# Optimization experiments

Hardware: AMD Instinct MI355X
Metric: run time of the kernel (lower is better)

Reference implementation:

```python
import jax, jax.numpy as jnp
import numpy as np

NODE_TYPES = ('user', 'vn', 'tag', 'staff', 'producer', 'character', 'trait')
N = {'user': 100000, 'vn': 40000, 'tag': 3000, 'staff': 20000, 'producer': 8000, 'character': 60000, 'trait': 3000}
# (src_type, dst_type) per edge type, in HGATConfig.edge_types order
EDGE_TYPES = (('user','vn'), ('vn','user'), ('vn','tag'), ('tag','vn'), ('vn','staff'), ('staff','vn'),
              ('vn','staff'), ('staff','vn'), ('vn','producer'), ('producer','vn'), ('vn','character'),
              ('character','vn'), ('character','trait'), ('trait','character'))
E_COUNTS = (1000000, 1000000, 500000, 500000, 200000, 200000, 200000, 200000, 100000, 100000, 300000, 300000, 400000, 400000)
HID = 128
LAYERS = 3
# number of edge types targeting each node type (HeteroConv aggr='mean' divisor)
NUM_DST = {'user': 1, 'vn': 6, 'tag': 1, 'staff': 2, 'producer': 1, 'character': 2, 'trait': 1}


def _l2norm(x):
    n = jnp.linalg.norm(x, axis=-1, keepdims=True)
    return x / jnp.maximum(n, 1e-12)


def _layernorm(x, g, b):
    m = jnp.mean(x, axis=-1, keepdims=True)
    v = jnp.mean((x - m) ** 2, axis=-1, keepdims=True)
    return (x - m) * jax.lax.rsqrt(v + 1e-5) * g + b


def _forward(xs, Wp, bp, Wl, bl, Wr, ln_g, ln_b, Wu, bu, Wv, bv, eis):
    # input projection per node type
    h = {t: xs[t] @ Wp[i].T + bp[i] for i, t in enumerate(NODE_TYPES)}
    # inverse in-degree per edge type (constant across layers)
    inv_deg = []
    for e, (st, dt) in enumerate(EDGE_TYPES):
        dst = eis[e][1]
        deg = jax.ops.segment_sum(jnp.ones(dst.shape[0], jnp.float32), dst, num_segments=N[dt])
        inv_deg.append(1.0 / jnp.maximum(deg, 1.0))
    for l in range(LAYERS):
        acc = {t: jnp.zeros((N[t], HID), h[t].dtype) for t in NODE_TYPES}
        for e, (st, dt) in enumerate(EDGE_TYPES):
            src, dst = eis[e][0], eis[e][1]
            # SAGEConv: mean-aggregate neighbor feats, then lin_l(agg) + lin_r(root), L2-normalize
            agg = jax.ops.segment_sum(h[st][src], dst, num_segments=N[dt]) * inv_deg[e][:, None]
            out = agg @ Wl[l, e].T + bl[l, e] + h[dt] @ Wr[l, e].T
            acc[dt] = acc[dt] + _l2norm(out)
        new_h = {}
        for i, t in enumerate(NODE_TYPES):
            x = acc[t] / NUM_DST[t] + h[t]  # HeteroConv mean over edge types + residual
            new_h[t] = jax.nn.relu(_layernorm(x, ln_g[l, i], ln_b[l, i]))  # dropout = identity (eval)
        h = new_h
    user_emb = _l2norm(h['user'] @ Wu.T + bu)
    vn_emb = _l2norm(h['vn'] @ Wv.T + bv)
    return user_emb, vn_emb


def setup_inputs() -> dict:
    key = jax.random.key(0)
    ks = iter(jax.random.split(key, 80))
    inp = {}
    for t in NODE_TYPES:
        inp['x_' + t] = jax.random.normal(next(ks), (N[t], HID), jnp.float32)
    for e, (st, dt) in enumerate(EDGE_TYPES):
        src = jax.random.randint(next(ks), (E_COUNTS[e],), 0, N[st], jnp.int32)
        dst = jax.random.randint(next(ks), (E_COUNTS[e],), 0, N[dt], jnp.int32)
        inp['ei_%d' % e] = jnp.stack([src, dst])
    s = 1.0 / np.sqrt(HID)
    inp['Wp'] = jax.random.normal(next(ks), (7, HID, HID), jnp.float32) * s
    inp['bp'] = jnp.zeros((7, HID), jnp.float32)
    inp['Wl'] = jax.random.normal(next(ks), (LAYERS, 14, HID, HID), jnp.float32) * s
    inp['bl'] = jnp.zeros((LAYERS, 14, HID), jnp.float32)
    inp['Wr'] = jax.random.normal(next(ks), (LAYERS, 14, HID, HID), jnp.float32) * s
    inp['ln_g'] = jnp.ones((LAYERS, 7, HID), jnp.float32)
    inp['ln_b'] = jnp.zeros((LAYERS, 7, HID), jnp.float32)
    inp['Wu'] = jax.random.normal(next(ks), (HID, HID), jnp.float32) * s
    inp['bu'] = jnp.zeros((HID,), jnp.float32)
    inp['Wv'] = jax.random.normal(next(ks), (HID, HID), jnp.float32) * s
    inp['bv'] = jnp.zeros((HID,), jnp.float32)
    return inp


def reference(x_user, x_vn, x_tag, x_staff, x_producer, x_character, x_trait,
              ei_0, ei_1, ei_2, ei_3, ei_4, ei_5, ei_6, ei_7, ei_8, ei_9, ei_10, ei_11, ei_12, ei_13,
              Wp, bp, Wl, bl, Wr, ln_g, ln_b, Wu, bu, Wv, bv):
    xs = {'user': x_user, 'vn': x_vn, 'tag': x_tag, 'staff': x_staff,
          'producer': x_producer, 'character': x_character, 'trait': x_trait}
    eis = [ei_0, ei_1, ei_2, ei_3, ei_4, ei_5, ei_6, ei_7, ei_8, ei_9, ei_10, ei_11, ei_12, ei_13]
    return _forward(xs, Wp, bp, Wl, bl, Wr, ln_g, ln_b, Wu, bu, Wv, bv, eis)
```

## Files before the change

### kernel.cpp

```cpp
#include <hip/hip_runtime.h>
#include <math.h>

#define TOTE 5400000
#define TOTN 234000
#define TOTC 514000
#define HID  128

#define NBUK 499
#define NBLK 1024


typedef __attribute__((ext_vector_type(8))) short short8;
typedef __attribute__((ext_vector_type(8))) __bf16 bf16x8;
typedef __attribute__((ext_vector_type(4))) float floatx4;
typedef __attribute__((ext_vector_type(2))) float float2v;

__constant__ int c_EPRE[15]   = {0,1000000,2000000,2500000,3000000,3200000,3400000,3600000,3800000,3900000,4000000,4300000,4600000,5000000,5400000};
__constant__ int c_ECNT[14]   = {1000000,1000000,500000,500000,200000,200000,200000,200000,100000,100000,300000,300000,400000,400000};
__constant__ int c_CNTOFF[14] = {0,40000,140000,143000,183000,203000,243000,263000,303000,311000,351000,411000,451000,454000};
__constant__ int c_CNTN[14]   = {40000,100000,3000,40000,20000,40000,20000,40000,8000,40000,60000,40000,3000,60000};
__constant__ int c_SRCOFF[14] = {0,100000,100000,140000,100000,143000,100000,143000,100000,163000,100000,171000,171000,231000};
__constant__ int c_NODEPRE[8] = {0,100000,140000,143000,163000,171000,231000,234000};
__constant__ int c_BSH[14]   = {9,10,6,10,10,11,10,11,10,11,11,11,6,11};
__constant__ int c_BBASE[15] = {0,79,177,224,264,284,304,324,344,352,372,402,422,469,499};

static __device__ __forceinline__ unsigned short f2bf(float f) {
    unsigned u = __float_as_uint(f);
    u = u + 0x7FFFu + ((u >> 16) & 1u);
    return (unsigned short)(u >> 16);
}
static __device__ __forceinline__ float bf2f(unsigned short s) {
    return __uint_as_float(((unsigned)s) << 16);
}

struct EdgeArgs { const int* ei[14]; };


__global__ __launch_bounds__(256) void hist_k(EdgeArgs a, int* __restrict__ blkHist) {
    __shared__ int h[NBUK];
    int t = threadIdx.x;
    for (int i = t; i < NBUK; i += 256) h[i] = 0;
    __syncthreads();
    const int per = (TOTE + NBLK - 1) / NBLK;
    int s = blockIdx.x * per;
    int eEnd = min(s + per, TOTE);
    for (int g = s + t; g < eEnd; g += 256) {
        int e = 0;
        while (g >= c_EPRE[e + 1]) e++;
        int k = g - c_EPRE[e];
        int dst = a.ei[e][c_ECNT[e] + k];
        atomicAdd(&h[c_BBASE[e] + (dst >> c_BSH[e])], 1);
    }
    __syncthreads();
    for (int i = t; i < NBUK; i += 256) blkHist[(size_t)i * NBLK + blockIdx.x] = h[i];
}

__global__ __launch_bounds__(256) void scan_blk_k(int* __restrict__ blkHist, int* __restrict__ bktCnt) {
    int b = blockIdx.x;
    int* p = blkHist + (size_t)b * NBLK;
    int t = threadIdx.x;
    int4 v = *(int4*)&p[t * 4];
    int s = v.x + v.y + v.z + v.w;
    int lane = t & 63, w = t >> 6;
    __shared__ int wt[4];
    int incl = s;
    #pragma unroll
    for (int d = 1; d < 64; d <<= 1) { int o = __shfl_up(incl, d); if (lane >= d) incl += o; }
    if (lane == 63) wt[w] = incl;
    __syncthreads();
    int wb = 0;
    for (int i = 0; i < w; i++) wb += wt[i];
    int excl = incl - s + wb;
    int4 o;
    o.x = excl; o.y = excl + v.x; o.z = excl + v.x + v.y; o.w = excl + v.x + v.y + v.z;
    *(int4*)&p[t * 4] = o;
    if (t == 255) bktCnt[b] = excl + s;
}

__global__ __launch_bounds__(512) void scans2_k(const int* __restrict__ bktCnt, int* __restrict__ bktEdgeBase) {
    int t = threadIdx.x;
    int v = (t < NBUK) ? bktCnt[t] : 0;
    int lane = t & 63, w = t >> 6;
    __shared__ int wt[8];
    int incl = v;
    #pragma unroll
    for (int d = 1; d < 64; d <<= 1) { int o = __shfl_up(incl, d); if (lane >= d) incl += o; }
    if (lane == 63) wt[w] = incl;
    __syncthreads();
    int wb = 0;
    for (int i = 0; i < w; i++) wb += wt[i];
    int excl = incl - v + wb;
    if (t < NBUK) bktEdgeBase[t] = excl;
    if (t == NBUK - 1) bktEdgeBase[NBUK] = excl + v;
}

__global__ __launch_bounds__(256) void scatter_k(EdgeArgs a, const int* __restrict__ blkHist,
        const int* __restrict__ bktEdgeBase, unsigned* __restrict__ pool) {
    __shared__ int cur[NBUK];
    int t = threadIdx.x;
    for (int i = t; i < NBUK; i += 256)
        cur[i] = bktEdgeBase[i] + blkHist[(size_t)i * NBLK + blockIdx.x];
    __syncthreads();
    const int per = (TOTE + NBLK - 1) / NBLK;
    int s = blockIdx.x * per;
    int eEnd = min(s + per, TOTE);
    for (int g = s + t; g < eEnd; g += 256) {
        int e = 0;
        while (g >= c_EPRE[e + 1]) e++;
        int k = g - c_EPRE[e];
        int src = a.ei[e][k];
        int dst = a.ei[e][c_ECNT[e] + k];
        int sh = c_BSH[e];
        unsigned rec = ((unsigned)(dst & ((1 << sh) - 1)) << 18) | (unsigned)(c_SRCOFF[e] + src);
        int p = atomicAdd(&cur[c_BBASE[e] + (dst >> sh)], 1);
        pool[p] = rec;
    }
}

__global__ __launch_bounds__(256) void csrfill_k(
        const unsigned* __restrict__ pool, const int* __restrict__ bktEdgeBase,
        int* __restrict__ cnt, int* __restrict__ cursor, float* __restrict__ invdeg,
        int* __restrict__ col) {
    __shared__ int hist[2048];
    __shared__ int cur[2048];
    __shared__ int wtot[4];
    __shared__ int wbase[4];
    int b = blockIdx.x;
    int t = threadIdx.x;
    int e = 0;
    while (b >= c_BBASE[e + 1]) e++;
    int lb = b - c_BBASE[e];
    int sh = c_BSH[e];
    int s0t = lb << sh;
    int span = min(1 << sh, c_CNTN[e] - s0t);
    int gs0 = c_CNTOFF[e] + s0t;
    int ebase = bktEdgeBase[b];
    int nrec = bktEdgeBase[b + 1] - ebase;

    for (int i = t; i < span; i += 256) hist[i] = 0;
    __syncthreads();
    for (int i = t; i < nrec; i += 256) atomicAdd(&hist[pool[ebase + i] >> 18], 1);
    __syncthreads();
    int base = t * 8, loc = 0, lv[8];
    #pragma unroll
    for (int i = 0; i < 8; i++) {
        int ii = base + i;
        int v = (ii < span) ? hist[ii] : 0;
        lv[i] = loc; loc += v;
    }
    int lane = t & 63, w = t >> 6;
    int incl = loc;
    #pragma unroll
    for (int d = 1; d < 64; d <<= 1) { int o = __shfl_up(incl, d); if (lane >= d) incl += o; }
    if (lane == 63) wtot[w] = incl;
    __syncthreads();
    if (t == 0) { int s2 = 0; for (int i = 0; i < 4; i++) { wbase[i] = s2; s2 += wtot[i]; } }
    __syncthreads();
    int texcl = incl - loc + wbase[w];
    #pragma unroll
    for (int i = 0; i < 8; i++) {
        int ii = base + i;
        if (ii < span) cur[ii] = texcl + lv[i];
    }
    __syncthreads();
    for (int i = t; i < span; i += 256) {
        int c = hist[i];
        cnt[gs0 + i] = c;
        cursor[gs0 + i] = ebase + cur[i] + c;
        invdeg[gs0 + i] = 1.0f / fmaxf((float)c, 1.0f);
    }
    __syncthreads();
    for (int i = t; i < nrec; i += 256) {
        unsigned rec = pool[ebase + i];
        int p = atomicAdd(&cur[rec >> 18], 1);
        col[ebase + p] = (int)(rec & 0x3FFFFu);
    }
}

struct XArgs { const float* x[7]; };
__global__ __launch_bounds__(256) void convx_k(XArgs a, unsigned short* __restrict__ hbf) {
    int i4 = blockIdx.x * 256 + threadIdx.x;
    if (i4 >= TOTN * 32) return;
    int idx = i4 * 4;
    int t = 0;
    while (idx >= c_NODEPRE[t + 1] * 128) t++;
    float4 v = *(const float4*)&a.x[t][idx - c_NODEPRE[t] * 128];
    uint2 p;
    p.x = (unsigned)f2bf(v.x) | ((unsigned)f2bf(v.y) << 16);
    p.y = (unsigned)f2bf(v.z) | ((unsigned)f2bf(v.w) << 16);
    *(uint2*)&hbf[idx] = p;
}

struct WArgs { const float* Wp; const float* Wl; const float* Wr; const float* Wu; const float* Wv; };
__global__ __launch_bounds__(256) void convw_k(WArgs a, unsigned short* __restrict__ wbf) {
    int i4 = blockIdx.x * 256 + threadIdx.x;
    if (i4 >= 93 * 4096) return;
    int idx = i4 * 4;
    int m = idx >> 14;
    int i = idx & 16383;
    const float* src;
    if (m < 7)       src = a.Wp + (size_t)m * 16384;
    else if (m < 49) src = a.Wl + (size_t)(m - 7) * 16384;
    else if (m < 91) src = a.Wr + (size_t)(m - 49) * 16384;
    else if (m == 91) src = a.Wu;
    else              src = a.Wv;
    float4 v = *(const float4*)&src[i];
    uint2 p;
    p.x = (unsigned)f2bf(v.x) | ((unsigned)f2bf(v.y) << 16);
    p.y = (unsigned)f2bf(v.z) | ((unsigned)f2bf(v.w) << 16);
    *(uint2*)&wbf[idx] = p;
}

#define ACC8v(u) do { \
    v01 += (float2v){__uint_as_float((u).x << 16), __uint_as_float((u).x & 0xFFFF0000u)}; \
    v23 += (float2v){__uint_as_float((u).y << 16), __uint_as_float((u).y & 0xFFFF0000u)}; \
    v45 += (float2v){__uint_as_float((u).z << 16), __uint_as_float((u).z & 0xFFFF0000u)}; \
    v67 += (float2v){__uint_as_float((u).w << 16), __uint_as_float((u).w & 0xFFFF0000u)}; } while (0)

__global__ __launch_bounds__(256) void agg_k(
        const int* __restrict__ cnt, const int* __restrict__ cursor,
        const float* __restrict__ inv_deg, const int* __restrict__ col,
        const unsigned short* __restrict__ hbf, unsigned short* __restrict__ slotb) {
    int row = blockIdx.x * 4 + (threadIdx.x >> 6);
    if (row >= TOTC) return;
    int lane = threadIdx.x & 63;
    int q = lane >> 4, li = lane & 15;
    int nn = cnt[row];
    int rs = cursor[row] - nn;
    const int* cp = col + rs;
    float2v v01 = {0.f, 0.f}, v23 = {0.f, 0.f}, v45 = {0.f, 0.f}, v67 = {0.f, 0.f};
    int j = 0;
    if (j + 8 <= nn) {
        int c0 = cp[q], c1 = cp[4 + q];
        for (; j + 8 <= nn; ) {
            int jn = j + 8;
            int n0 = 0, n1 = 0;
            if (jn + 8 <= nn) { n0 = cp[jn + q]; n1 = cp[jn + 4 + q]; }
            uint4 u0 = *(const uint4*)&hbf[(c0 << 7) + li * 8];
            uint4 u1 = *(const uint4*)&hbf[(c1 << 7) + li * 8];
            ACC8v(u0);
            ACC8v(u1);
            c0 = n0; c1 = n1; j = jn;
        }
    }
    for (; j < nn; j += 4) {
        if (j + q < nn) {
            int c = cp[j + q] << 7;
            uint4 u = *(const uint4*)&hbf[c + li * 8];
            ACC8v(u);
        }
    }
    float inv = inv_deg[row];
    float v[8] = {v01.x, v01.y, v23.x, v23.y, v45.x, v45.y, v67.x, v67.y};
    #pragma unroll
    for (int i = 0; i < 8; i++) {
        v[i] += __shfl_xor(v[i], 16);
        v[i] += __shfl_xor(v[i], 32);
        v[i] *= inv;
    }
    if (q == 0) {
        uint4 o;
        o.x = (unsigned)f2bf(v[0]) | ((unsigned)f2bf(v[1]) << 16);
        o.y = (unsigned)f2bf(v[2]) | ((unsigned)f2bf(v[3]) << 16);
        o.z = (unsigned)f2bf(v[4]) | ((unsigned)f2bf(v[5]) << 16);
        o.w = (unsigned)f2bf(v[6]) | ((unsigned)f2bf(v[7]) << 16);
        *(uint4*)&slotb[(size_t)row * HID + li * 8] = o;
    }
}

struct FusArgs {
    int blockPrefix[8];
    int ns[7];
    int a1off[7][6];
    const unsigned short* W1[7][6];
    const unsigned short* W2[7][6];
    const float* bias[7][6];
    int nodepre[7];
    int nrows[7];
    float invnd[7];
};

__global__ __launch_bounds__(256) void fusedln_k(FusArgs g,
        unsigned short* __restrict__ hbf, const unsigned short* __restrict__ slotb,
        const float* __restrict__ ln_g, const float* __restrict__ ln_b, int l) {
    __shared__ short As2[64 * 168];
    __shared__ short A1c[64 * 40];
    __shared__ short W1c[128 * 40];
    __shared__ short W2c[128 * 40];
    int b = blockIdx.x;
    int t = 0;
    while (b >= g.blockPrefix[t + 1]) t++;
    int nrows = g.nrows[t];
    int row0 = (b - g.blockPrefix[t]) * 64;
    int dst0 = g.nodepre[t] + row0;
    int tid = threadIdx.x;
    int w = tid >> 6, lane = tid & 63;
    int q = lane >> 4, m15 = lane & 15;

    {
        const uint4* h4 = (const uint4*)hbf;
        #pragma unroll
        for (int it = 0; it < 4; it++) {
            int c = tid + it * 256;
            int row = c >> 4, kc = c & 15;
            uint4 v = make_uint4(0u, 0u, 0u, 0u);
            if (row0 + row < nrows) v = h4[(size_t)(dst0 + row) * 16 + kc];
            *(uint4*)&As2[row * 168 + (kc >> 2) * 40 + (kc & 3) * 8] = v;
        }
    }

    floatx4 accsum[8];
    #pragma unroll
    for (int bb = 0; bb < 8; bb++) accsum[bb] = (floatx4){0.f, 0.f, 0.f, 0.f};

    int ns = g.ns[t];
    for (int ei = 0; ei < ns; ei++) {
        const uint4* A14 = (const uint4*)(slotb + (size_t)g.a1off[t][ei] * HID);
        const uint4* W14 = (const uint4*)g.W1[t][ei];
        const uint4* W24 = (const uint4*)g.W2[t][ei];
        floatx4 acc[8];
        #pragma unroll
        for (int bb = 0; bb < 8; bb++) acc[bb] = (floatx4){0.f, 0.f, 0.f, 0.f};
        for (int k0 = 0; k0 < 4; k0++) {
            __syncthreads();
            {
                int row = tid >> 2, kc = tid & 3;
                uint4 v = make_uint4(0u, 0u, 0u, 0u);
                if (row0 + row < nrows) v = A14[(size_t)(row0 + row) * 16 + k0 * 4 + kc];
                *(uint4*)&A1c[row * 40 + kc * 8] = v;
            }
            #pragma unroll
            for (int i = 0; i < 2; i++) {
                int idx = tid + i * 256;
                int c = idx >> 2, kc = idx & 3;
                *(uint4*)&W1c[c * 40 + kc * 8] = W14[(size_t)c * 16 + k0 * 4 + kc];
                *(uint4*)&W2c[c * 40 + kc * 8] = W24[(size_t)c * 16 + k0 * 4 + kc];
            }
            __syncthreads();
            bf16x8 a1 = __builtin_bit_cast(bf16x8, *(const short8*)&A1c[(w * 16 + m15) * 40 + q * 8]);
            bf16x8 a2 = __builtin_bit_cast(bf16x8, *(const short8*)&As2[(w * 16 + m15) * 168 + k0 * 40 + q * 8]);
            #pragma unroll
            for (int bb = 0; bb < 8; bb++) {
                bf16x8 w1 = __builtin_bit_cast(bf16x8, *(const short8*)&W1c[(bb * 16 + m15) * 40 + q * 8]);
                bf16x8 w2 = __builtin_bit_cast(bf16x8, *(const short8*)&W2c[(bb * 16 + m15) * 40 + q * 8]);
                acc[bb] = __builtin_amdgcn_mfma_f32_16x16x32_bf16(a1, w1, acc[bb], 0, 0, 0);
                acc[bb] = __builtin_amdgcn_mfma_f32_16x16x32_bf16(a2, w2, acc[bb], 0, 0, 0);
            }
        }
        const float* bias = g.bias[t][ei];
        #pragma unroll
        for (int bb = 0; bb < 8; bb++) {
            float bv = bias[bb * 16 + m15];
            #pragma unroll
            for (int reg = 0; reg < 4; reg++) acc[bb][reg] += bv;
        }
        #pragma unroll
        for (int reg = 0; reg < 4; reg++) {
            float ss = 0.f;
            #pragma unroll
            for (int bb = 0; bb < 8; bb++) ss += acc[bb][reg] * acc[bb][reg];
            ss += __shfl_xor(ss, 1);
            ss += __shfl_xor(ss, 2);
            ss += __shfl_xor(ss, 4);
            ss += __shfl_xor(ss, 8);
            float sc = 1.0f / fmaxf(sqrtf(ss), 1e-12f);
            #pragma unroll
            for (int bb = 0; bb < 8; bb++) accsum[bb][reg] += acc[bb][reg] * sc;
        }
    }

    float invnd = g.invnd[t];
    const float* gg = ln_g + ((size_t)l * 7 + t) * HID;
    const float* bbp = ln_b + ((size_t)l * 7 + t) * HID;
    float gv[8], bv2[8];
    #pragma unroll
    for (int bb = 0; bb < 8; bb++) {
        gv[bb]  = gg[bb * 16 + m15];
        bv2[bb] = bbp[bb * 16 + m15];
    }
    #pragma unroll
    for (int reg = 0; reg < 4; reg++) {
        int lrow = w * 16 + q * 4 + reg;
        float x[8];
        #pragma unroll
        for (int bb = 0; bb < 8; bb++) {
            float resid = bf2f((unsigned short)As2[lrow * 168 + (bb >> 1) * 40 + (bb & 1) * 16 + m15]);
            x[bb] = accsum[bb][reg] * invnd + resid;
        }
        float s = 0.f;
        #pragma unroll
        for (int bb = 0; bb < 8; bb++) s += x[bb];
        s += __shfl_xor(s, 1);
        s += __shfl_xor(s, 2);
        s += __shfl_xor(s, 4);
        s += __shfl_xor(s, 8);
        float mean = s * (1.0f / 128.0f);
        float vs = 0.f;
        #pragma unroll
        for (int bb = 0; bb < 8; bb++) { float d = x[bb] - mean; vs += d * d; }
        vs += __shfl_xor(vs, 1);
        vs += __shfl_xor(vs, 2);
        vs += __shfl_xor(vs, 4);
        vs += __shfl_xor(vs, 8);
        float rstd = rsqrtf(vs * (1.0f / 128.0f) + 1e-5f);
        if (row0 + lrow < nrows) {
            unsigned short* o = hbf + (size_t)(dst0 + lrow) * HID;
            #pragma unroll
            for (int bb = 0; bb < 8; bb++) {
                float y = (x[bb] - mean) * rstd * gv[bb] + bv2[bb];
                o[bb * 16 + m15] = f2bf(fmaxf(y, 0.f));
            }
        }
    }
}

struct GemmArgs {
    int blockPrefix[15];
    const unsigned short* A1[14];
    const unsigned short* W1[14];
    const float* bias[14]; void* out[14];
    int rows[14];
};

template<int MODE>
__global__ __launch_bounds__(256) void gemm_k(GemmArgs g) {
    __shared__ short As[64 * 40];
    __shared__ short Ws[128 * 40];
    int b = blockIdx.x;
    int s = 0;
    while (b >= g.blockPrefix[s + 1]) s++;
    int rows = g.rows[s];
    int row0 = (b - g.blockPrefix[s]) * 64;
    int t = threadIdx.x;
    int w = t >> 6, lane = t & 63;
    int q = lane >> 4, m15 = lane & 15;

    floatx4 acc[8];
    #pragma unroll
    for (int bb = 0; bb < 8; bb++) acc[bb] = (floatx4){0.f, 0.f, 0.f, 0.f};

    const uint4* A4 = (const uint4*)g.A1[s];
    const uint4* W4 = (const uint4*)g.W1[s];
    for (int k0 = 0; k0 < 128; k0 += 32) {
        __syncthreads();
        {
            int row = t >> 2, kc = t & 3;
            uint4 v = make_uint4(0u, 0u, 0u, 0u);
            if (row0 + row < rows) v = A4[(size_t)(row0 + row) * 16 + (k0 >> 3) + kc];
            *(uint4*)&As[row * 40 + kc * 8] = v;
        }
        #pragma unroll
        for (int i = 0; i < 2; i++) {
            int idx = t + i * 256;
            int c = idx >> 2, kc = idx & 3;
            uint4 v = W4[(size_t)c * 16 + (k0 >> 3) + kc];
            *(uint4*)&Ws[c * 40 + kc * 8] = v;
        }
        __syncthreads();
        bf16x8 af = __builtin_bit_cast(bf16x8, *(const short8*)&As[(w * 16 + m15) * 40 + q * 8]);
        #pragma unroll
        for (int bb = 0; bb < 8; bb++) {
            bf16x8 bf = __builtin_bit_cast(bf16x8, *(const short8*)&Ws[(bb * 16 + m15) * 40 + q * 8]);
            acc[bb] = __builtin_amdgcn_mfma_f32_16x16x32_bf16(af, bf, acc[bb], 0, 0, 0);
        }
    }

    const float* bias = g.bias[s];
    #pragma unroll
    for (int bb = 0; bb < 8; bb++) {
        float bv = bias[bb * 16 + m15];
        #pragma unroll
        for (int reg = 0; reg < 4; reg++) acc[bb][reg] += bv;
    }
    if (MODE != 0) {
        #pragma unroll
        for (int reg = 0; reg < 4; reg++) {
            float ss = 0.f;
            #pragma unroll
            for (int bb = 0; bb < 8; bb++) ss += acc[bb][reg] * acc[bb][reg];
            ss += __shfl_xor(ss, 1);
            ss += __shfl_xor(ss, 2);
            ss += __shfl_xor(ss, 4);
            ss += __shfl_xor(ss, 8);
            float sc = 1.0f / fmaxf(sqrtf(ss), 1e-12f);
            #pragma unroll
            for (int bb = 0; bb < 8; bb++) acc[bb][reg] *= sc;
        }
    }
    int rbase = row0 + w * 16 + q * 4;
    if (MODE == 3) {
        float* out = (float*)g.out[s];
        #pragma unroll
        for (int reg = 0; reg < 4; reg++) {
            int r = rbase + reg;
            if (r < rows) {
                float* o = out + (size_t)r * HID;
                #pragma unroll
                for (int bb = 0; bb < 8; bb++) o[bb * 16 + m15] = acc[bb][reg];
            }
        }
    } else {
        unsigned short* out = (unsigned short*)g.out[s];
        #pragma unroll
        for (int reg = 0; reg < 4; reg++) {
            int r = rbase + reg;
            if (r < rows) {
                unsigned short* o = out + (size_t)r * HID;
                #pragma unroll
                for (int bb = 0; bb < 8; bb++) o[bb * 16 + m15] = f2bf(acc[bb][reg]);
            }
        }
    }
}

extern "C" void kernel_launch(void* const* d_in, const int* in_sizes, int n_in,
                              void* d_out, int out_size, void* d_ws, size_t ws_size,
                              hipStream_t stream) {
    (void)in_sizes; (void)n_in; (void)out_size; (void)ws_size;
    const float* Wp   = (const float*)d_in[21];
    const float* bp   = (const float*)d_in[22];
    const float* bl   = (const float*)d_in[24];
    const float* ln_g = (const float*)d_in[26];
    const float* ln_b = (const float*)d_in[27];
    const float* bu   = (const float*)d_in[29];
    const float* bv   = (const float*)d_in[31];
    float* out = (float*)d_out;

    unsigned short* h_bf   = (unsigned short*)d_ws;
    unsigned short* w_bf   = h_bf + (size_t)TOTN * HID;
    unsigned short* slotb  = w_bf + (size_t)93 * 16384;
    int*            cnt    = (int*)(slotb + (size_t)TOTC * HID);
    int*            cursor = cnt + TOTC;
    float*          invdeg = (float*)(cursor + TOTC);
    unsigned*       pool   = (unsigned*)(invdeg + TOTC);
    int*            blkHist = (int*)(pool + (size_t)TOTE);
    int*            ctrl    = blkHist + (size_t)NBUK * NBLK;
    int* bktCnt       = ctrl;
    int* bktEdgeBase  = ctrl + NBUK;

    int* col = (int*)d_out;

    static const int CNTOFF[14] = {0,40000,140000,143000,183000,203000,243000,263000,303000,311000,351000,411000,451000,454000};
    static const int NODEPRE[8] = {0,100000,140000,143000,163000,171000,231000,234000};
    static const int NT[7]      = {100000,40000,3000,20000,8000,60000,3000};
    static const int FEED_NS[7] = {1,6,1,2,1,2,1};
    static const int FEED_E[7][6] = {
        {1,0,0,0,0,0},
        {0,3,5,7,9,11},
        {2,0,0,0,0,0},
        {4,6,0,0,0,0},
        {8,0,0,0,0,0},
        {10,13,0,0,0,0},
        {12,0,0,0,0,0}};
    static const float INVND[7] = {1.0f, 1.0f/6.0f, 1.0f, 0.5f, 1.0f, 0.5f, 1.0f};

    EdgeArgs ea;
    for (int e = 0; e < 14; e++) ea.ei[e] = (const int*)d_in[7 + e];

    hist_k<<<NBLK, 256, 0, stream>>>(ea, blkHist);
    scan_blk_k<<<NBUK, 256, 0, stream>>>(blkHist, bktCnt);
    scans2_k<<<1, 512, 0, stream>>>(bktCnt, bktEdgeBase);
    scatter_k<<<NBLK, 256, 0, stream>>>(ea, blkHist, bktEdgeBase, pool);
    csrfill_k<<<NBUK, 256, 0, stream>>>(pool, bktEdgeBase, cnt, cursor, invdeg, col);

    {
        XArgs xa;
        for (int t = 0; t < 7; t++) xa.x[t] = (const float*)d_in[t];
        convx_k<<<(TOTN * 32 + 255) / 256, 256, 0, stream>>>(xa, h_bf);
        WArgs wa = {Wp, (const float*)d_in[23], (const float*)d_in[25],
                    (const float*)d_in[28], (const float*)d_in[30]};
        convw_k<<<(93 * 4096 + 255) / 256, 256, 0, stream>>>(wa, w_bf);
    }

    {
        GemmArgs ga;
        int pre = 0; ga.blockPrefix[0] = 0;
        for (int t = 0; t < 7; t++) {
            ga.A1[t] = h_bf + (size_t)NODEPRE[t] * HID;
            ga.W1[t] = w_bf + (size_t)t * 16384;
            ga.bias[t] = bp + (size_t)t * HID;
            ga.out[t] = h_bf + (size_t)NODEPRE[t] * HID;
            ga.rows[t] = NT[t];
            pre += (NT[t] + 63) / 64;
            ga.blockPrefix[t + 1] = pre;
        }
        for (int s = 7; s < 14; s++) { ga.blockPrefix[s + 1] = pre; ga.rows[s] = 0; }
        gemm_k<0><<<pre, 256, 0, stream>>>(ga);
    }

    FusArgs fa;
    int fgrid;
    {
        int pre = 0; fa.blockPrefix[0] = 0;
        for (int t = 0; t < 7; t++) {
            fa.ns[t] = FEED_NS[t];
            fa.nodepre[t] = NODEPRE[t];
            fa.nrows[t] = NT[t];
            fa.invnd[t] = INVND[t];
            for (int j = 0; j < 6; j++) fa.a1off[t][j] = CNTOFF[FEED_E[t][j]];
            pre += (NT[t] + 63) / 64;
            fa.blockPrefix[t + 1] = pre;
        }
        fgrid = pre;
    }
    for (int l = 0; l < 3; l++) {
        agg_k<<<(TOTC + 3) / 4, 256, 0, stream>>>(cnt, cursor, invdeg, col, h_bf, slotb);
        for (int t = 0; t < 7; t++) {
            for (int j = 0; j < 6; j++) {
                int e = FEED_E[t][j];
                fa.W1[t][j]   = w_bf + (size_t)(7  + l * 14 + e) * 16384;
                fa.W2[t][j]   = w_bf + (size_t)(49 + l * 14 + e) * 16384;
                fa.bias[t][j] = bl + ((size_t)l * 14 + e) * HID;
            }
        }
        fusedln_k<<<fgrid, 256, 0, stream>>>(fa, h_bf, slotb, ln_g, ln_b, l);
    }

    {
        GemmArgs ga;
        ga.blockPrefix[0] = 0;
        ga.A1[0] = h_bf;
        ga.W1[0] = w_bf + (size_t)91 * 16384;
        ga.bias[0] = bu;                        ga.out[0] = out;
        ga.rows[0] = 100000;
        ga.blockPrefix[1] = (100000 + 63) / 64;
        ga.A1[1] = h_bf + (size_t)100000 * HID;
        ga.W1[1] = w_bf + (size_t)92 * 16384;
        ga.bias[1] = bv;                        ga.out[1] = out + (size_t)100000 * HID;
        ga.rows[1] = 40000;
        int tot = ga.blockPrefix[1] + (40000 + 63) / 64;
        for (int s = 2; s < 14; s++) { ga.blockPrefix[s + 1] = tot; ga.rows[s] = 0; }
        ga.blockPrefix[2] = tot;
        gemm_k<3><<<tot, 256, 0, stream>>>(ga);
    }
}
```

Baseline: 1.500 ms.

## Assign one 16-lane group per aggregation row instead of a full wavefront

The aggregation kernel now maps each destination row to 16 threads instead of 64, so each wavefront handles four rows. Each thread loops over every neighbor serially with a 4-way unrolled gather, which removes the cross-quarter shuffle reduction and the idle lanes on the store. Rows with many neighbors (e.g. user→vn has an average of about 25 edges per vn) now take longer per group and can cause imbalance within a wavefront. Low-degree rows no longer leave three-quarters of the lanes idle.

```diff
diff --git a/kernel.cpp b/kernel.cpp
--- a/kernel.cpp
+++ b/kernel.cpp
@@ -221,51 +221,41 @@
         const int* __restrict__ cnt, const int* __restrict__ cursor,
         const float* __restrict__ inv_deg, const int* __restrict__ col,
         const unsigned short* __restrict__ hbf, unsigned short* __restrict__ slotb) {
-    int row = blockIdx.x * 4 + (threadIdx.x >> 6);
+    int row = blockIdx.x * 16 + (threadIdx.x >> 4);
     if (row >= TOTC) return;
-    int lane = threadIdx.x & 63;
-    int q = lane >> 4, li = lane & 15;
+    int li = threadIdx.x & 15;
     int nn = cnt[row];
     int rs = cursor[row] - nn;
     const int* cp = col + rs;
     float2v v01 = {0.f, 0.f}, v23 = {0.f, 0.f}, v45 = {0.f, 0.f}, v67 = {0.f, 0.f};
     int j = 0;
-    if (j + 8 <= nn) {
-        int c0 = cp[q], c1 = cp[4 + q];
-        for (; j + 8 <= nn; ) {
-            int jn = j + 8;
-            int n0 = 0, n1 = 0;
-            if (jn + 8 <= nn) { n0 = cp[jn + q]; n1 = cp[jn + 4 + q]; }
-            uint4 u0 = *(const uint4*)&hbf[(c0 << 7) + li * 8];
-            uint4 u1 = *(const uint4*)&hbf[(c1 << 7) + li * 8];
-            ACC8v(u0);
-            ACC8v(u1);
-            c0 = n0; c1 = n1; j = jn;
-        }
-    }
-    for (; j < nn; j += 4) {
-        if (j + q < nn) {
-            int c = cp[j + q] << 7;
-            uint4 u = *(const uint4*)&hbf[c + li * 8];
-            ACC8v(u);
-        }
+    for (; j + 4 <= nn; j += 4) {
+        int c0 = cp[j]     << 7;
+        int c1 = cp[j + 1] << 7;
+        int c2 = cp[j + 2] << 7;
+        int c3 = cp[j + 3] << 7;
+        uint4 u0 = *(const uint4*)&hbf[c0 + li * 8];
+        uint4 u1 = *(const uint4*)&hbf[c1 + li * 8];
+        uint4 u2 = *(const uint4*)&hbf[c2 + li * 8];
+        uint4 u3 = *(const uint4*)&hbf[c3 + li * 8];
+        ACC8v(u0);
+        ACC8v(u1);
+        ACC8v(u2);
+        ACC8v(u3);
+    }
+    for (; j < nn; j++) {
+        int c = cp[j] << 7;
+        uint4 u = *(const uint4*)&hbf[c + li * 8];
+        ACC8v(u);
     }
     float inv = inv_deg[row];
     float v[8] = {v01.x, v01.y, v23.x, v23.y, v45.x, v45.y, v67.x, v67.y};
-    #pragma unroll
-    for (int i = 0; i < 8; i++) {
-        v[i] += __shfl_xor(v[i], 16);
-        v[i] += __shfl_xor(v[i], 32);
-        v[i] *= inv;
-    }
-    if (q == 0) {
-        uint4 o;
-        o.x = (unsigned)f2bf(v[0]) | ((unsigned)f2bf(v[1]) << 16);
-        o.y = (unsigned)f2bf(v[2]) | ((unsigned)f2bf(v[3]) << 16);
-        o.z = (unsigned)f2bf(v[4]) | ((unsigned)f2bf(v[5]) << 16);
-        o.w = (unsigned)f2bf(v[6]) | ((unsigned)f2bf(v[7]) << 16);
-        *(uint4*)&slotb[(size_t)row * HID + li * 8] = o;
-    }
+    uint4 o;
+    o.x = (unsigned)f2bf(v[0] * inv) | ((unsigned)f2bf(v[1] * inv) << 16);
+    o.y = (unsigned)f2bf(v[2] * inv) | ((unsigned)f2bf(v[3] * inv) << 16);
+    o.z = (unsigned)f2bf(v[4] * inv) | ((unsigned)f2bf(v[5] * inv) << 16);
+    o.w = (unsigned)f2bf(v[6] * inv) | ((unsigned)f2bf(v[7] * inv) << 16);
+    *(uint4*)&slotb[(size_t)row * HID + li * 8] = o;
 }
 
 struct FusArgs {
@@ -604,7 +594,7 @@
         fgrid = pre;
     }
     for (int l = 0; l < 3; l++) {
-        agg_k<<<(TOTC + 3) / 4, 256, 0, stream>>>(cnt, cursor, invdeg, col, h_bf, slotb);
+        agg_k<<<(TOTC + 15) / 16, 256, 0, stream>>>(cnt, cursor, invdeg, col, h_bf, slotb);
         for (int t = 0; t < 7; t++) {
             for (int j = 0; j < 6; j++) {
                 int e = FEED_E[t][j];
```

Result: faster. 1.345 ms (-10.3%).
